# Optimization experiments

Hardware: AMD Instinct MI355X
Metric: run time of the kernel (lower is better)

Reference implementation:

```python
import jax, jax.numpy as jnp
import numpy as np

N_NODES = 50000
N_EDGES = 600000
IN_DIM = 128
HID_DIM = 512
OUT_DIM = 2


def setup_inputs() -> dict:
    key = jax.random.key(0)
    ks = jax.random.split(key, 8)
    x = jax.random.normal(ks[0], (N_NODES, IN_DIM), dtype=jnp.float32)
    edge_index = jax.random.randint(ks[1], (2, N_EDGES), 0, N_NODES, dtype=jnp.int32)
    s1 = 1.0 / np.sqrt(IN_DIM)
    s2 = 1.0 / np.sqrt(HID_DIM)
    # SAGEConv params: lin_l (applied to mean-aggregated neighbors, has bias),
    # lin_r (applied to root node features, no bias)
    W1l = jax.random.uniform(ks[2], (IN_DIM, HID_DIM), jnp.float32, -s1, s1)
    b1 = jax.random.uniform(ks[3], (HID_DIM,), jnp.float32, -s1, s1)
    W1r = jax.random.uniform(ks[4], (IN_DIM, HID_DIM), jnp.float32, -s1, s1)
    W2l = jax.random.uniform(ks[5], (HID_DIM, OUT_DIM), jnp.float32, -s2, s2)
    b2 = jax.random.uniform(ks[6], (OUT_DIM,), jnp.float32, -s2, s2)
    W2r = jax.random.uniform(ks[7], (HID_DIM, OUT_DIM), jnp.float32, -s2, s2)
    return {"x": x, "W1l": W1l, "b1": b1, "W1r": W1r,
            "W2l": W2l, "b2": b2, "W2r": W2r, "edge_index": edge_index}


def _sage_conv(x, edge_index, Wl, b, Wr):
    src, dst = edge_index[0], edge_index[1]
    msgs = x[src]                                             # [E, d]
    agg = jax.ops.segment_sum(msgs, dst, num_segments=x.shape[0])  # [N, d]
    deg = jax.ops.segment_sum(jnp.ones_like(dst, dtype=x.dtype), dst,
                              num_segments=x.shape[0])
    agg = agg / jnp.maximum(deg, 1.0)[:, None]                # mean aggregation
    return agg @ Wl + b + x @ Wr


def reference(x, W1l, b1, W1r, W2l, b2, W2r, edge_index):
    h = _sage_conv(x, edge_index, W1l, b1, W1r)
    h = jax.nn.relu(h)
    # dropout inactive (eval mode / force_dropout=False)
    out = _sage_conv(h, edge_index, W2l, b2, W2r)
    return jax.nn.log_softmax(out, axis=1)
```

## Files before the change

### kernel.cpp

```cpp
#include <hip/hip_runtime.h>
#include <math.h>
#include <stdint.h>

#define N_NODES 50000
#define N_EDGES 600000
#define IN_DIM 128
#define HID_DIM 512
#define M_PAD 50048
#define SCAN_NB 196

#define CASTX_NB 6250
#define DEG_NB   2344
#define CASTW_NB 544

typedef __bf16 bf16;
typedef __bf16 bf16x2 __attribute__((ext_vector_type(2)));
typedef __bf16 bf16x4 __attribute__((ext_vector_type(4)));
typedef __bf16 bf16x8 __attribute__((ext_vector_type(8)));
typedef float f32x4 __attribute__((ext_vector_type(4)));

#define GLDS(gp, lp) __builtin_amdgcn_global_load_lds( \
    (const __attribute__((address_space(1))) uint32_t*)(gp), \
    (__attribute__((address_space(3))) uint32_t*)(lp), 16, 0, 0)


__global__ __launch_bounds__(256) void prep_kernel(
    const float* __restrict__ x, bf16* __restrict__ xb,
    const int* __restrict__ dst, int* __restrict__ deg,
    const float* __restrict__ W1l, const float* __restrict__ W1r,
    const float* __restrict__ W2l, const float* __restrict__ W2r,
    bf16* __restrict__ Wt, bf16* __restrict__ W2bt) {
    int b = blockIdx.x;
    int t = threadIdx.x;
    if (b < CASTX_NB) {
        int i = b * 256 + t;
        float4 v = ((const float4*)x)[i];
        bf16x4 o = {(bf16)v.x, (bf16)v.y, (bf16)v.z, (bf16)v.w};
        *(bf16x4*)(xb + (size_t)i * 4) = o;
    } else if (b < CASTX_NB + DEG_NB) {
        int i = (b - CASTX_NB) * 256 + t;
        if (i < N_EDGES) atomicAdd(&deg[dst[i]], 1);
    } else {
        int idx = (b - CASTX_NB - DEG_NB) * 256 + t;
        if (idx < 512 * 256) {
            int n = idx >> 8;
            int k = idx & 255;
            float v = (k < IN_DIM) ? W1l[(size_t)k * HID_DIM + n]
                                   : W1r[(size_t)(k - IN_DIM) * HID_DIM + n];
            Wt[idx] = (bf16)v;
        } else {
            int j = idx - 512 * 256;
            int n = j >> 9;
            int k = j & 511;
            float v = 0.f;
            if (n == 0) v = W2l[k * 2 + 0];
            else if (n == 1) v = W2l[k * 2 + 1];
            else if (n == 2) v = W2r[k * 2 + 0];
            else if (n == 3) v = W2r[k * 2 + 1];
            W2bt[j] = (bf16)v;
        }
    }
}


__global__ __launch_bounds__(256) void scan1_kernel(const int* __restrict__ deg,
                                                    int* __restrict__ bsum) {
    int t = threadIdx.x;
    int i = blockIdx.x * 256 + t;
    int v = (i < N_NODES) ? deg[i] : 0;
#pragma unroll
    for (int m = 1; m < 64; m <<= 1) v += __shfl_xor(v, m);
    __shared__ int ws_[4];
    int w = t >> 6, l = t & 63;
    if (l == 0) ws_[w] = v;
    __syncthreads();
    if (t == 0) bsum[blockIdx.x] = ws_[0] + ws_[1] + ws_[2] + ws_[3];
}

__global__ __launch_bounds__(256) void scan3_kernel(const int* __restrict__ deg,
                                                    const int* __restrict__ bsum,
                                                    int* __restrict__ offsets,
                                                    int* __restrict__ cursor) {
    int t = threadIdx.x;
    int blk = blockIdx.x;
    int i = blk * 256 + t;
    int l = t & 63, w = t >> 6;
    int v = (i < N_NODES) ? deg[i] : 0;
    int inc = v;
#pragma unroll
    for (int off = 1; off < 64; off <<= 1) {
        int y = __shfl_up(inc, off);
        if (l >= off) inc += y;
    }
    __shared__ int wsum[4];
    __shared__ int lookback;
    if (l == 63) wsum[w] = inc;
    __syncthreads();
    if (t < 64) {
        int s = 0;
        for (int u = t; u < blk; u += 64) s += bsum[u];
#pragma unroll
        for (int m = 1; m < 64; m <<= 1) s += __shfl_xor(s, m);
        if (t == 0) lookback = s;
    }
    __syncthreads();
    int add = lookback;
    for (int u = 0; u < w; ++u) add += wsum[u];
    int ex = add + inc - v;
    if (i < N_NODES) { offsets[i] = ex; cursor[i] = ex; }
    if (blk == 0 && t == 0) offsets[N_NODES] = N_EDGES;
}

__global__ void csr_fill_kernel(const int* __restrict__ src, const int* __restrict__ dst,
                                int* __restrict__ cursor, int* __restrict__ csr_src) {
    int i = blockIdx.x * blockDim.x + threadIdx.x;
    if (i < N_EDGES) {
        int p = atomicAdd(&cursor[dst[i]], 1);
        csr_src[p] = src[i];
    }
}


__global__ __launch_bounds__(256) void agg1_kernel(
    const bf16* __restrict__ xb, const int* __restrict__ offsets,
    const int* __restrict__ csr_src, bf16* __restrict__ agg1b) {
    int t = threadIdx.x;
    int w = t >> 6, l = t & 63;
    int g = l >> 4;
    int sl = l & 15;
    int n = blockIdx.x * 16 + w * 4 + g;
    int s0 = offsets[n], s1 = offsets[n + 1];
    float a[8] = {};
    int e = s0;
    for (; e + 4 <= s1; e += 4) {
        int i0 = csr_src[e + 0];
        int i1 = csr_src[e + 1];
        int i2 = csr_src[e + 2];
        int i3 = csr_src[e + 3];
        bf16x8 v0 = *(const bf16x8*)(xb + (size_t)i0 * IN_DIM + sl * 8);
        bf16x8 v1 = *(const bf16x8*)(xb + (size_t)i1 * IN_DIM + sl * 8);
        bf16x8 v2 = *(const bf16x8*)(xb + (size_t)i2 * IN_DIM + sl * 8);
        bf16x8 v3 = *(const bf16x8*)(xb + (size_t)i3 * IN_DIM + sl * 8);
#pragma unroll
        for (int u = 0; u < 8; ++u)
            a[u] += (float)v0[u] + (float)v1[u] + (float)v2[u] + (float)v3[u];
    }
    for (; e < s1; ++e) {
        int i0 = csr_src[e];
        bf16x8 v0 = *(const bf16x8*)(xb + (size_t)i0 * IN_DIM + sl * 8);
#pragma unroll
        for (int u = 0; u < 8; ++u) a[u] += (float)v0[u];
    }
    float inv = 1.0f / fmaxf((float)(s1 - s0), 1.0f);
    bf16x8 o;
#pragma unroll
    for (int u = 0; u < 8; ++u) o[u] = (bf16)(a[u] * inv);
    *(bf16x8*)(agg1b + (size_t)n * IN_DIM + sl * 8) = o;
}


__global__ __launch_bounds__(256) void gemm1_kernel(
    const bf16* __restrict__ agg1b, const bf16* __restrict__ xb,
    const bf16* __restrict__ Wt, const float* __restrict__ b1,
    const bf16* __restrict__ W2bt, float* __restrict__ zpart) {
    __shared__ __align__(16) char smem[128 * 136 * 2];
    bf16 (*As)[128][32] = (bf16(*)[128][32])smem;
    bf16 (*Bs)[128][32] = (bf16(*)[128][32])(smem + 16384);
    bf16 (*Hs)[136] = (bf16(*)[136])smem;
    int tid = threadIdx.x;
    int w = tid >> 6;
    int lane = tid & 63;
    int q = lane >> 4, rr = lane & 15;
    int cb = blockIdx.x;
    int n0 = cb * 128;
    int row0 = blockIdx.y * 128;
    int wm = (w & 1) * 64, wn = (w >> 1) * 64;
    int lr = lane >> 2;
    int lc = (lane & 3) * 8;

    auto stage = [&](int ki) {
        const bf16* Asrc;
        int kb;
        if (ki < 4) { Asrc = agg1b; kb = ki * 32; }
        else        { Asrc = xb;    kb = ki * 32 - IN_DIM; }
        int kw = ki * 32;
        int buf = ki & 1;
#pragma unroll
        for (int j = 0; j < 2; ++j) {
            int r = w * 32 + j * 16 + lr;
            GLDS(Asrc + (size_t)(row0 + r) * IN_DIM + kb + lc,
                 &As[buf][w * 32 + j * 16][0]);
            GLDS(Wt + (size_t)(n0 + r) * 256 + kw + lc,
                 &Bs[buf][w * 32 + j * 16][0]);
        }
    };

    f32x4 acc[4][4] = {};
    stage(0);
#pragma unroll
    for (int ki = 0; ki < 8; ++ki) {
        __syncthreads();
        if (ki + 1 < 8) stage(ki + 1);
        int buf = ki & 1;
        bf16x8 af[4], bfr[4];
#pragma unroll
        for (int i = 0; i < 4; ++i)
            af[i] = *(const bf16x8*)&As[buf][wm + i * 16 + rr][q * 8];
#pragma unroll
        for (int j = 0; j < 4; ++j)
            bfr[j] = *(const bf16x8*)&Bs[buf][wn + j * 16 + rr][q * 8];
#pragma unroll
        for (int i = 0; i < 4; ++i)
#pragma unroll
            for (int j = 0; j < 4; ++j)
                acc[i][j] = __builtin_amdgcn_mfma_f32_16x16x32_bf16(
                    af[i], bfr[j], acc[i][j], 0, 0, 0);
    }
    __syncthreads();
    float bias[4];
#pragma unroll
    for (int j = 0; j < 4; ++j) bias[j] = b1[n0 + wn + j * 16 + rr];
#pragma unroll
    for (int i = 0; i < 4; ++i) {
#pragma unroll
        for (int rg = 0; rg < 4; ++rg) {
            int mrow = wm + i * 16 + q * 4 + rg;
#pragma unroll
            for (int j = 0; j < 4; ++j)
                Hs[mrow][wn + j * 16 + rr] =
                    (bf16)fmaxf(acc[i][j][rg] + bias[j], 0.f);
        }
    }
    __syncthreads();
    bf16x8 wf[4];
#pragma unroll
    for (int ks = 0; ks < 4; ++ks)
        wf[ks] = *(const bf16x8*)(W2bt + (size_t)rr * 512 + n0 + ks * 32 + q * 8);
    f32x4 zacc[2] = {};
#pragma unroll
    for (int mt = 0; mt < 2; ++mt)
#pragma unroll
        for (int ks = 0; ks < 4; ++ks) {
            bf16x8 afz = *(const bf16x8*)&Hs[w * 32 + mt * 16 + rr][ks * 32 + q * 8];
            zacc[mt] = __builtin_amdgcn_mfma_f32_16x16x32_bf16(
                afz, wf[ks], zacc[mt], 0, 0, 0);
        }
    if (rr < 4) {
#pragma unroll
        for (int mt = 0; mt < 2; ++mt)
#pragma unroll
            for (int rg = 0; rg < 4; ++rg) {
                int grow = row0 + w * 32 + mt * 16 + q * 4 + rg;
                zpart[(size_t)grow * 16 + cb * 4 + rr] = zacc[mt][rg];
            }
    }
}


__global__ __launch_bounds__(256) void zsum_kernel(const float* __restrict__ zpart,
                                                   float* __restrict__ z) {
    int n = blockIdx.x * blockDim.x + threadIdx.x;
    if (n >= N_NODES) return;
    const float4* p = (const float4*)(zpart + (size_t)n * 16);
    float4 a = p[0], b = p[1], c = p[2], d = p[3];
    float4 o = {a.x + b.x + c.x + d.x, a.y + b.y + c.y + d.y,
                a.z + b.z + c.z + d.z, a.w + b.w + c.w + d.w};
    *(float4*)(z + (size_t)n * 4) = o;
}


__global__ void final_kernel(const float* __restrict__ z, const int* __restrict__ offsets,
                             const int* __restrict__ csr_src, const float* __restrict__ b2,
                             float* __restrict__ out) {
    int n = blockIdx.x * blockDim.x + threadIdx.x;
    if (n >= N_NODES) return;
    int s0 = offsets[n], s1 = offsets[n + 1];
    float a0 = 0.f, a1 = 0.f;
    int e = s0;
    for (; e + 4 <= s1; e += 4) {
        int i0 = csr_src[e], i1 = csr_src[e + 1];
        int i2 = csr_src[e + 2], i3 = csr_src[e + 3];
        float2 v0 = *(const float2*)(z + (size_t)i0 * 4);
        float2 v1 = *(const float2*)(z + (size_t)i1 * 4);
        float2 v2 = *(const float2*)(z + (size_t)i2 * 4);
        float2 v3 = *(const float2*)(z + (size_t)i3 * 4);
        a0 += v0.x + v1.x + v2.x + v3.x;
        a1 += v0.y + v1.y + v2.y + v3.y;
    }
    for (; e < s1; ++e) {
        int s = csr_src[e];
        float2 v = *(const float2*)(z + (size_t)s * 4);
        a0 += v.x;
        a1 += v.y;
    }
    float inv = 1.0f / fmaxf((float)(s1 - s0), 1.0f);
    float2 zs = *(const float2*)(z + (size_t)n * 4 + 2);
    float o0 = a0 * inv + b2[0] + zs.x;
    float o1 = a1 * inv + b2[1] + zs.y;
    float m = fmaxf(o0, o1);
    float lse = logf(expf(o0 - m) + expf(o1 - m));
    float2 o = {o0 - m - lse, o1 - m - lse};
    *(float2*)(out + (size_t)n * 2) = o;
}


extern "C" void kernel_launch(void* const* d_in, const int* in_sizes, int n_in,
                              void* d_out, int out_size, void* d_ws, size_t ws_size,
                              hipStream_t stream) {
    const float* x   = (const float*)d_in[0];
    const float* W1l = (const float*)d_in[1];
    const float* b1  = (const float*)d_in[2];
    const float* W1r = (const float*)d_in[3];
    const float* W2l = (const float*)d_in[4];
    const float* b2  = (const float*)d_in[5];
    const float* W2r = (const float*)d_in[6];
    const int* edge  = (const int*)d_in[7];
    const int* src = edge;
    const int* dst = edge + N_EDGES;
    float* out = (float*)d_out;

    char* ws = (char*)d_ws;
    size_t off = 0;
    auto alloc = [&](size_t bytes) -> void* {
        void* p = ws + off;
        off += (bytes + 255) & ~(size_t)255;
        return p;
    };
    int* deg     = (int*)alloc((size_t)N_NODES * 4);
    int* offsets = (int*)alloc((size_t)(N_NODES + 1) * 4);
    int* cursor  = (int*)alloc((size_t)N_NODES * 4);
    int* csr_src = (int*)alloc((size_t)N_EDGES * 4);
    int* bsum    = (int*)alloc((size_t)SCAN_NB * 4);
    bf16* xb     = (bf16*)alloc((size_t)M_PAD * IN_DIM * 2);
    bf16* agg1b  = (bf16*)alloc((size_t)M_PAD * IN_DIM * 2);
    bf16* Wt     = (bf16*)alloc((size_t)HID_DIM * 256 * 2);
    bf16* W2bt   = (bf16*)alloc((size_t)16 * HID_DIM * 2);
    float* zpart = (float*)alloc((size_t)M_PAD * 16 * 4);
    float* z     = (float*)alloc((size_t)N_NODES * 4 * 4);

    hipMemsetAsync(deg, 0, (size_t)N_NODES * 4, stream);
    prep_kernel<<<CASTX_NB + DEG_NB + CASTW_NB, 256, 0, stream>>>(
        x, xb, dst, deg, W1l, W1r, W2l, W2r, Wt, W2bt);
    scan1_kernel<<<SCAN_NB, 256, 0, stream>>>(deg, bsum);
    scan3_kernel<<<SCAN_NB, 256, 0, stream>>>(deg, bsum, offsets, cursor);
    csr_fill_kernel<<<(N_EDGES + 255) / 256, 256, 0, stream>>>(src, dst, cursor, csr_src);
    agg1_kernel<<<N_NODES / 16, 256, 0, stream>>>(xb, offsets, csr_src, agg1b);
    gemm1_kernel<<<dim3(4, M_PAD / 128), 256, 0, stream>>>(
        agg1b, xb, Wt, b1, W2bt, zpart);
    zsum_kernel<<<(N_NODES + 255) / 256, 256, 0, stream>>>(zpart, z);
    final_kernel<<<(N_NODES + 255) / 256, 256, 0, stream>>>(z, offsets, csr_src, b2, out);
}
```

Measured before the change: 206.6 us.

## Widen per-thread work in prep, CSR fill, aggregation and final kernels

The x cast and degree count now handle two elements per thread with wider loads. The CSR fill processes edge pairs with int2 loads. agg1 unrolls the gather to 8 neighbors to keep more loads in flight, and final_kernel gives each node 8 lanes that split its edges and combine with a shuffle reduction. The goal is more memory-level parallelism and fewer launched threads. In exchange, register pressure rises and many final-kernel lanes sit idle on low-degree nodes.

```diff
diff --git a/kernel.cpp b/kernel.cpp
--- a/kernel.cpp
+++ b/kernel.cpp
@@ -9,8 +9,8 @@
 #define M_PAD 50048
 #define SCAN_NB 196
 
-#define CASTX_NB 6250
-#define DEG_NB   2344
+#define CASTX_NB 3125
+#define DEG_NB   1172
 #define CASTW_NB 544
 
 typedef __bf16 bf16;
@@ -34,12 +34,20 @@
     int t = threadIdx.x;
     if (b < CASTX_NB) {
         int i = b * 256 + t;
-        float4 v = ((const float4*)x)[i];
-        bf16x4 o = {(bf16)v.x, (bf16)v.y, (bf16)v.z, (bf16)v.w};
-        *(bf16x4*)(xb + (size_t)i * 4) = o;
+        float4 v0 = ((const float4*)x)[2 * i];
+        float4 v1 = ((const float4*)x)[2 * i + 1];
+        bf16x8 o = {(bf16)v0.x, (bf16)v0.y, (bf16)v0.z, (bf16)v0.w,
+                    (bf16)v1.x, (bf16)v1.y, (bf16)v1.z, (bf16)v1.w};
+        *(bf16x8*)(xb + (size_t)i * 8) = o;
     } else if (b < CASTX_NB + DEG_NB) {
-        int i = (b - CASTX_NB) * 256 + t;
-        if (i < N_EDGES) atomicAdd(&deg[dst[i]], 1);
+        int e = ((b - CASTX_NB) * 256 + t) * 2;
+        if (e + 1 < N_EDGES) {
+            int2 d2 = *(const int2*)(dst + e);
+            atomicAdd(&deg[d2.x], 1);
+            atomicAdd(&deg[d2.y], 1);
+        } else if (e < N_EDGES) {
+            atomicAdd(&deg[dst[e]], 1);
+        }
     } else {
         int idx = (b - CASTX_NB - DEG_NB) * 256 + t;
         if (idx < 512 * 256) {
@@ -113,10 +121,17 @@
 
 __global__ void csr_fill_kernel(const int* __restrict__ src, const int* __restrict__ dst,
                                 int* __restrict__ cursor, int* __restrict__ csr_src) {
-    int i = blockIdx.x * blockDim.x + threadIdx.x;
-    if (i < N_EDGES) {
-        int p = atomicAdd(&cursor[dst[i]], 1);
-        csr_src[p] = src[i];
+    int e = (blockIdx.x * blockDim.x + threadIdx.x) * 2;
+    if (e + 1 < N_EDGES) {
+        int2 s2 = *(const int2*)(src + e);
+        int2 d2 = *(const int2*)(dst + e);
+        int p0 = atomicAdd(&cursor[d2.x], 1);
+        csr_src[p0] = s2.x;
+        int p1 = atomicAdd(&cursor[d2.y], 1);
+        csr_src[p1] = s2.y;
+    } else if (e < N_EDGES) {
+        int p = atomicAdd(&cursor[dst[e]], 1);
+        csr_src[p] = src[e];
     }
 }
 
@@ -132,29 +147,43 @@
     int s0 = offsets[n], s1 = offsets[n + 1];
     float a[8] = {};
     int e = s0;
-    for (; e + 4 <= s1; e += 4) {
-        int i0 = csr_src[e + 0];
-        int i1 = csr_src[e + 1];
-        int i2 = csr_src[e + 2];
-        int i3 = csr_src[e + 3];
-        bf16x8 v0 = *(const bf16x8*)(xb + (size_t)i0 * IN_DIM + sl * 8);
-        bf16x8 v1 = *(const bf16x8*)(xb + (size_t)i1 * IN_DIM + sl * 8);
-        bf16x8 v2 = *(const bf16x8*)(xb + (size_t)i2 * IN_DIM + sl * 8);
-        bf16x8 v3 = *(const bf16x8*)(xb + (size_t)i3 * IN_DIM + sl * 8);
+    for (; e + 8 <= s1; e += 8) {
+        int idx[8];
+#pragma unroll
+        for (int u = 0; u < 8; ++u) idx[u] = csr_src[e + u];
+        bf16x8 v[8];
 #pragma unroll
         for (int u = 0; u < 8; ++u)
-            a[u] += (float)v0[u] + (float)v1[u] + (float)v2[u] + (float)v3[u];
+            v[u] = *(const bf16x8*)(xb + (size_t)idx[u] * IN_DIM + sl * 8);
+#pragma unroll
+        for (int u = 0; u < 8; ++u)
+#pragma unroll
+            for (int c = 0; c < 8; ++c) a[c] += (float)v[u][c];
+    }
+    if (e + 4 <= s1) {
+        int idx[4];
+#pragma unroll
+        for (int u = 0; u < 4; ++u) idx[u] = csr_src[e + u];
+        bf16x8 v[4];
+#pragma unroll
+        for (int u = 0; u < 4; ++u)
+            v[u] = *(const bf16x8*)(xb + (size_t)idx[u] * IN_DIM + sl * 8);
+#pragma unroll
+        for (int u = 0; u < 4; ++u)
+#pragma unroll
+            for (int c = 0; c < 8; ++c) a[c] += (float)v[u][c];
+        e += 4;
     }
     for (; e < s1; ++e) {
         int i0 = csr_src[e];
         bf16x8 v0 = *(const bf16x8*)(xb + (size_t)i0 * IN_DIM + sl * 8);
 #pragma unroll
-        for (int u = 0; u < 8; ++u) a[u] += (float)v0[u];
+        for (int c = 0; c < 8; ++c) a[c] += (float)v0[c];
     }
     float inv = 1.0f / fmaxf((float)(s1 - s0), 1.0f);
     bf16x8 o;
 #pragma unroll
-    for (int u = 0; u < 8; ++u) o[u] = (bf16)(a[u] * inv);
+    for (int c = 0; c < 8; ++c) o[c] = (bf16)(a[c] * inv);
     *(bf16x8*)(agg1b + (size_t)n * IN_DIM + sl * 8) = o;
 }
 
@@ -269,38 +298,40 @@
 }
 
 
-__global__ void final_kernel(const float* __restrict__ z, const int* __restrict__ offsets,
-                             const int* __restrict__ csr_src, const float* __restrict__ b2,
-                             float* __restrict__ out) {
-    int n = blockIdx.x * blockDim.x + threadIdx.x;
-    if (n >= N_NODES) return;
-    int s0 = offsets[n], s1 = offsets[n + 1];
+__global__ __launch_bounds__(256) void final_kernel(
+    const float* __restrict__ z, const int* __restrict__ offsets,
+    const int* __restrict__ csr_src, const float* __restrict__ b2,
+    float* __restrict__ out) {
+    int t = threadIdx.x;
+    int w = t >> 6, l = t & 63;
+    int g = l >> 3;
+    int sl = l & 7;
+    int n = blockIdx.x * 32 + w * 8 + g;
+    bool valid = (n < N_NODES);
+    int s0 = valid ? offsets[n] : 0;
+    int s1 = valid ? offsets[n + 1] : 0;
     float a0 = 0.f, a1 = 0.f;
-    int e = s0;
-    for (; e + 4 <= s1; e += 4) {
-        int i0 = csr_src[e], i1 = csr_src[e + 1];
-        int i2 = csr_src[e + 2], i3 = csr_src[e + 3];
-        float2 v0 = *(const float2*)(z + (size_t)i0 * 4);
-        float2 v1 = *(const float2*)(z + (size_t)i1 * 4);
-        float2 v2 = *(const float2*)(z + (size_t)i2 * 4);
-        float2 v3 = *(const float2*)(z + (size_t)i3 * 4);
-        a0 += v0.x + v1.x + v2.x + v3.x;
-        a1 += v0.y + v1.y + v2.y + v3.y;
-    }
-    for (; e < s1; ++e) {
+    for (int e = s0 + sl; e < s1; e += 8) {
         int s = csr_src[e];
         float2 v = *(const float2*)(z + (size_t)s * 4);
         a0 += v.x;
         a1 += v.y;
     }
-    float inv = 1.0f / fmaxf((float)(s1 - s0), 1.0f);
-    float2 zs = *(const float2*)(z + (size_t)n * 4 + 2);
-    float o0 = a0 * inv + b2[0] + zs.x;
-    float o1 = a1 * inv + b2[1] + zs.y;
-    float m = fmaxf(o0, o1);
-    float lse = logf(expf(o0 - m) + expf(o1 - m));
-    float2 o = {o0 - m - lse, o1 - m - lse};
-    *(float2*)(out + (size_t)n * 2) = o;
+#pragma unroll
+    for (int m = 1; m < 8; m <<= 1) {
+        a0 += __shfl_xor(a0, m);
+        a1 += __shfl_xor(a1, m);
+    }
+    if (valid && sl == 0) {
+        float inv = 1.0f / fmaxf((float)(s1 - s0), 1.0f);
+        float2 zs = *(const float2*)(z + (size_t)n * 4 + 2);
+        float o0 = a0 * inv + b2[0] + zs.x;
+        float o1 = a1 * inv + b2[1] + zs.y;
+        float m = fmaxf(o0, o1);
+        float lse = logf(expf(o0 - m) + expf(o1 - m));
+        float2 o = {o0 - m - lse, o1 - m - lse};
+        *(float2*)(out + (size_t)n * 2) = o;
+    }
 }
 
 
@@ -343,10 +374,11 @@
         x, xb, dst, deg, W1l, W1r, W2l, W2r, Wt, W2bt);
     scan1_kernel<<<SCAN_NB, 256, 0, stream>>>(deg, bsum);
     scan3_kernel<<<SCAN_NB, 256, 0, stream>>>(deg, bsum, offsets, cursor);
-    csr_fill_kernel<<<(N_EDGES + 255) / 256, 256, 0, stream>>>(src, dst, cursor, csr_src);
+    csr_fill_kernel<<<(N_EDGES / 2 + 255) / 256, 256, 0, stream>>>(
+        src, dst, cursor, csr_src);
     agg1_kernel<<<N_NODES / 16, 256, 0, stream>>>(xb, offsets, csr_src, agg1b);
     gemm1_kernel<<<dim3(4, M_PAD / 128), 256, 0, stream>>>(
         agg1b, xb, Wt, b1, W2bt, zpart);
     zsum_kernel<<<(N_NODES + 255) / 256, 256, 0, stream>>>(zpart, z);
-    final_kernel<<<(N_NODES + 255) / 256, 256, 0, stream>>>(z, offsets, csr_src, b2, out);
-}
+    final_kernel<<<(N_NODES + 31) / 32, 256, 0, stream>>>(z, offsets, csr_src, b2, out);
+}
```

New measurement: 209.7 us. About the same (+1.5%).
